# Kernel tuning notes

Hardware: AMD Instinct MI355X
Metric: run time of the kernel (lower is better)

Reference implementation:

```python
import jax, jax.numpy as jnp
import numpy as np

EPS = 1e-12  # F.normalize eps

def _l2norm(v, axis):
    n = jnp.sqrt(jnp.sum(v * v, axis=axis, keepdims=True))
    return v / jnp.maximum(n, EPS)

def setup_inputs() -> dict:
    key = jax.random.key(0)
    k1, k2, k3 = jax.random.split(key, 3)
    B, C, H, W, K = 64, 128, 64, 64, 64
    x = jax.random.normal(k1, (B, C, H, W), dtype=jnp.float32)
    conv_w = jax.random.normal(k2, (K, C), dtype=jnp.float32) * 0.1  # 1x1 conv, no bias
    centroids = jax.random.uniform(k3, (K, C), dtype=jnp.float32)
    return {"x": x, "conv_w": conv_w, "centroids": centroids}

def reference(x, conv_w, centroids):
    B, C, H, W = x.shape
    K = conv_w.shape[0]
    x_flat = x.reshape(B, C, H * W)                     # [B,C,N]
    logits = jnp.einsum('kc,bcn->bkn', conv_w, x_flat)  # 1x1 conv
    a = jax.nn.softmax(logits, axis=1)                  # softmax over clusters
    # vlad[b,k,c] = sum_n a[b,k,n] * (x[b,c,n] - centroids[k,c])
    vlad = jnp.einsum('bkn,bcn->bkc', a, x_flat) - a.sum(axis=2)[:, :, None] * centroids[None]
    vlad = _l2norm(vlad, axis=2)          # intra-normalize per cluster
    vlad = vlad.reshape(B, K * C)
    vlad = _l2norm(vlad, axis=1)          # global L2 normalize
    return vlad
```

## Files before the change

### kernel.cpp

```cpp
#include <hip/hip_runtime.h>
#include <math.h>

#define BB 64
#define CC 128
#define KK 64
#define NN 4096
#define PCH 128
#define NCH 8
#define SLAB (PCH*NCH)
#define VSTRIDE ((size_t)BB*KK*CC)

typedef __attribute__((ext_vector_type(8))) short short8;
typedef __attribute__((ext_vector_type(16))) float f32x16;

__device__ __forceinline__ unsigned f2bf(float f) {
    unsigned u = __float_as_uint(f);
    return (u + 0x7fffu + ((u >> 16) & 1u)) >> 16;
}

__device__ __forceinline__ short8 pack8(float4 a, float4 b) {
    short8 r;
    r[0]=(short)f2bf(a.x); r[1]=(short)f2bf(a.y); r[2]=(short)f2bf(a.z); r[3]=(short)f2bf(a.w);
    r[4]=(short)f2bf(b.x); r[5]=(short)f2bf(b.y); r[6]=(short)f2bf(b.z); r[7]=(short)f2bf(b.w);
    return r;
}

#define LDS_FENCE_BARRIER() do {                                  \
    asm volatile("s_waitcnt lgkmcnt(0)" ::: "memory");            \
    __builtin_amdgcn_s_barrier();                                 \
} while (0)

__global__ __launch_bounds__(512, 2) void nv_phase1(
    const float* __restrict__ x,
    const float* __restrict__ convw,
    float* __restrict__ vlad,
    float* __restrict__ wsf)
{
    __shared__ alignas(16) unsigned short xs[PCH*CC];
    __shared__ alignas(16) unsigned short xc[CC*PCH];
    __shared__ float redsm[2][PCH];
    __shared__ float asred[2][2][16][4];

    unsigned short* al = xs;

    const int t  = threadIdx.x;
    const int b  = blockIdx.y;
    const int slab = blockIdx.x;
    const int n_slab = slab * SLAB;
    const int l   = t & 63;
    const int wid = t >> 6;
    const int ln  = l & 31;
    const int q   = l >> 5;
    const int kt  = wid & 1;
    const int nt  = wid >> 1;
    const int ct  = wid & 3;
    const int kt2 = wid >> 2;
    const int r4  = t & 3;

    const float* xb = x + (size_t)b * CC * NN;
    const int n_ = ln + 32*nt;
    const int c2 = ln + 32*ct;
    const int k2 = ln + 32*kt2;

    float4 pf[8];
#pragma unroll
    for (int i = 0; i < 8; ++i) {
        int u = (t >> 2) + 128 * i, cQ = u >> 5, nQ = u & 31;
        pf[i] = *(const float4*)(xb + (size_t)(4*cQ + r4) * NN + n_slab + 4*nQ);
    }

    short8 wfrag[8];
    {
        const float* wr = convw + (size_t)(ln + 32*kt) * CC + 8*q;
#pragma unroll
        for (int cs = 0; cs < 8; ++cs) {
            float4 a  = *(const float4*)(wr + 16*cs);
            float4 bb = *(const float4*)(wr + 16*cs + 4);
            wfrag[cs] = pack8(a, bb);
        }
    }

    f32x16 vacc;
#pragma unroll
    for (int i = 0; i < 16; ++i) vacc[i] = 0.f;
    float asum_l[16];
#pragma unroll
    for (int i = 0; i < 16; ++i) asum_l[i] = 0.f;

#pragma unroll 1
    for (int chk = 0; chk < NCH; ++chk) {
#pragma unroll
        for (int i = 0; i < 8; ++i) {
            int u = (t >> 2) + 128 * i, cQ = u >> 5, nQ = u & 31;
            unsigned d0 = f2bf(pf[i].x) | (f2bf(pf[i].y) << 16);
            unsigned d1 = f2bf(pf[i].z) | (f2bf(pf[i].w) << 16);
            int c = 4*cQ + r4;
            *(uint2*)((char*)xc + c*256 + ((((nQ >> 1) ^ (c & 7)) << 4) | ((nQ & 1) * 8)))
                = make_uint2(d0, d1);
            unsigned q0 = (unsigned)__shfl_xor((int)d0, 1);
            unsigned q1 = (unsigned)__shfl_xor((int)d1, 1);
            unsigned e, f;
            if (r4 & 1) { e = (q0 >> 16) | (d0 & 0xffff0000u);
                          f = (q1 >> 16) | (d1 & 0xffff0000u); }
            else        { e = (d0 & 0xffffu) | (q0 << 16);
                          f = (d1 & 0xffffu) | (q1 << 16); }
            unsigned s2 = (unsigned)__shfl_xor((int)((r4 & 2) ? e : f), 2);
            unsigned w0 = (r4 & 2) ? s2 : e;
            unsigned w1 = (r4 & 2) ? f : s2;
            int nn  = 4*nQ + r4;
            int chp = (cQ >> 1) ^ (nn & 7);
            *(uint2*)((char*)xs + nn*256 + (chp << 4) + (cQ & 1)*8) = make_uint2(w0, w1);
        }
        if (chk + 1 < NCH) {
            const int gn1 = n_slab + (chk + 1) * PCH;
#pragma unroll
            for (int i = 0; i < 8; ++i) {
                int u = (t >> 2) + 128 * i, cQ = u >> 5, nQ = u & 31;
                pf[i] = *(const float4*)(xb + (size_t)(4*cQ + r4) * NN + gn1 + 4*nQ);
            }
        }
        LDS_FENCE_BARRIER();

        f32x16 lacc;
#pragma unroll
        for (int i = 0; i < 16; ++i) lacc[i] = 0.f;
#pragma unroll
        for (int cs = 0; cs < 8; ++cs) {
            int chp = (2*cs + q) ^ (n_ & 7);
            short8 bf = *(const short8*)((const char*)xs + n_*256 + (chp << 4));
            lacc = __builtin_amdgcn_mfma_f32_32x32x16_bf16(wfrag[cs], bf, lacc, 0, 0, 0);
        }

        float ssum = 0.f;
#pragma unroll
        for (int i = 0; i < 16; ++i) { float e2 = __expf(lacc[i]); lacc[i] = e2; ssum += e2; }
        ssum += __shfl_xor(ssum, 32);
        if (q == 0) redsm[kt][n_] = ssum;
        LDS_FENCE_BARRIER();

        float inv = 1.0f / (redsm[0][n_] + redsm[1][n_]);
#pragma unroll
        for (int i = 0; i < 16; ++i) {
            float a = lacc[i] * inv;
            asum_l[i] += a;
            int k_ = 32*kt + 4*q + (i & 3) + 8*(i >> 2);
            al[k_*128 + ((((n_ >> 3) ^ (k_ & 7)) << 3) | (n_ & 7))] = (unsigned short)f2bf(a);
        }
        LDS_FENCE_BARRIER();

#pragma unroll
        for (int ns = 0; ns < 8; ++ns) {
            int ca = (2*ns + q) ^ (c2 & 7);
            short8 af = *(const short8*)((const char*)xc + c2*256 + (ca << 4));
            int cb = (2*ns + q) ^ (k2 & 7);
            short8 bf = *(const short8*)((const char*)al + k2*256 + (cb << 4));
            vacc = __builtin_amdgcn_mfma_f32_32x32x16_bf16(af, bf, vacc, 0, 0, 0);
        }
        LDS_FENCE_BARRIER();
    }

    {
        float* base = (slab == 0)
            ? vlad + (size_t)b * KK * CC
            : wsf + (size_t)(slab - 1) * VSTRIDE + (size_t)b * KK * CC;
        float* vb = base + (size_t)k2 * CC + 32*ct + 4*q;
#pragma unroll
        for (int g = 0; g < 4; ++g) {
            float4 o;
            o.x = vacc[4*g+0]; o.y = vacc[4*g+1]; o.z = vacc[4*g+2]; o.w = vacc[4*g+3];
            *(float4*)(vb + 8*g) = o;
        }
    }

#pragma unroll
    for (int i = 0; i < 16; ++i) {
        float v = asum_l[i];
        v += __shfl_xor(v, 1);  v += __shfl_xor(v, 2);  v += __shfl_xor(v, 4);
        v += __shfl_xor(v, 8);  v += __shfl_xor(v, 16);
        asum_l[i] = v;
    }
    if (ln == 0) {
#pragma unroll
        for (int i = 0; i < 16; ++i) asred[kt][q][i][nt] = asum_l[i];
    }
    __syncthreads();
    if (t < 64) {
        int kt_ = t >> 5, q_ = (t >> 4) & 1, r_ = t & 15;
        int k_ = 32*kt_ + 4*q_ + (r_ & 3) + 8*(r_ >> 2);
        float s = asred[kt_][q_][r_][0] + asred[kt_][q_][r_][1]
                + asred[kt_][q_][r_][2] + asred[kt_][q_][r_][3];
        wsf[3 * VSTRIDE + (size_t)slab * BB * KK + b * KK + k_] = s;
    }
}

__global__ __launch_bounds__(256) void nv_phase2(
    float* __restrict__ vlad,
    const float* __restrict__ wsf,
    const float* __restrict__ cent)
{
    __shared__ float gred[4];
    const int b    = blockIdx.x;
    const int w    = threadIdx.x >> 6;
    const int lane = threadIdx.x & 63;
    const float* ap = wsf + 3 * VSTRIDE;

    float v[32];
    float gsum = 0.f;
#pragma unroll
    for (int r = 0; r < 16; r++) {
        int k = w * 16 + r;
        float a = ap[0*BB*KK + b*KK + k] + ap[1*BB*KK + b*KK + k]
                + ap[2*BB*KK + b*KK + k] + ap[3*BB*KK + b*KK + k];
        size_t o = ((size_t)b * KK + k) * CC + lane;
        float x0 = vlad[o]      + wsf[o]      + wsf[VSTRIDE + o]      + wsf[2*VSTRIDE + o];
        float x1 = vlad[o + 64] + wsf[o + 64] + wsf[VSTRIDE + o + 64] + wsf[2*VSTRIDE + o + 64];
        x0 -= a * cent[k * CC + lane];
        x1 -= a * cent[k * CC + lane + 64];
        float ss = x0 * x0 + x1 * x1;
#pragma unroll
        for (int m = 1; m < 64; m <<= 1) ss += __shfl_xor(ss, m, 64);
        float rn = 1.0f / fmaxf(sqrtf(ss), 1e-12f);
        v[2 * r]     = x0 * rn;
        v[2 * r + 1] = x1 * rn;
        gsum += ss * rn * rn;
    }
    if (lane == 0) gred[w] = gsum;
    __syncthreads();
    float g  = gred[0] + gred[1] + gred[2] + gred[3];
    float gs = 1.0f / fmaxf(sqrtf(g), 1e-12f);
#pragma unroll
    for (int r = 0; r < 16; r++) {
        int k = w * 16 + r;
        vlad[((size_t)b * KK + k) * CC + lane]      = v[2 * r]     * gs;
        vlad[((size_t)b * KK + k) * CC + lane + 64] = v[2 * r + 1] * gs;
    }
}

extern "C" void kernel_launch(void* const* d_in, const int* in_sizes, int n_in,
                              void* d_out, int out_size, void* d_ws, size_t ws_size,
                              hipStream_t stream) {
    const float* x     = (const float*)d_in[0];
    const float* convw = (const float*)d_in[1];
    const float* cent  = (const float*)d_in[2];
    float* out = (float*)d_out;
    float* wsf = (float*)d_ws;

    nv_phase1<<<dim3(NN / SLAB, BB), 512, 0, stream>>>(x, convw, out, wsf);
    nv_phase2<<<BB, 256, 0, stream>>>(out, wsf, cent);
}
```

Measured before the change: 48.88 us.

## Halve slab length to double phase-1 blocks and fold assignment sums into MFMA loop

Each phase-1 block now covers half as many spatial chunks, so the grid has twice as many blocks (8 slabs per batch) and the occupancy hint is raised to 4 blocks per CU. The per-cluster assignment sums are no longer accumulated in registers and reduced through shared memory at the end; they are summed from the bf16 assignment fragments already loaded for the second MFMA. This removes the tail reduction and its barrier. In exchange there are more partial VLAD slabs written to and read back from the workspace in phase 2, and the assignment sums now come from bf16-rounded values.

```diff
diff --git a/kernel.cpp b/kernel.cpp
--- a/kernel.cpp
+++ b/kernel.cpp
@@ -6,8 +6,9 @@
 #define KK 64
 #define NN 4096
 #define PCH 128
-#define NCH 8
+#define NCH 4
 #define SLAB (PCH*NCH)
+#define NSLAB (NN/SLAB)
 #define VSTRIDE ((size_t)BB*KK*CC)
 
 typedef __attribute__((ext_vector_type(8))) short short8;
@@ -30,7 +31,7 @@
     __builtin_amdgcn_s_barrier();                                 \
 } while (0)
 
-__global__ __launch_bounds__(512, 2) void nv_phase1(
+__global__ __launch_bounds__(512, 4) void nv_phase1(
     const float* __restrict__ x,
     const float* __restrict__ convw,
     float* __restrict__ vlad,
@@ -39,7 +40,6 @@
     __shared__ alignas(16) unsigned short xs[PCH*CC];
     __shared__ alignas(16) unsigned short xc[CC*PCH];
     __shared__ float redsm[2][PCH];
-    __shared__ float asred[2][2][16][4];
 
     unsigned short* al = xs;
 
@@ -83,9 +83,7 @@
     f32x16 vacc;
 #pragma unroll
     for (int i = 0; i < 16; ++i) vacc[i] = 0.f;
-    float asum_l[16];
-#pragma unroll
-    for (int i = 0; i < 16; ++i) asum_l[i] = 0.f;
+    float asacc = 0.f;
 
 #pragma unroll 1
     for (int chk = 0; chk < NCH; ++chk) {
@@ -142,7 +140,6 @@
 #pragma unroll
         for (int i = 0; i < 16; ++i) {
             float a = lacc[i] * inv;
-            asum_l[i] += a;
             int k_ = 32*kt + 4*q + (i & 3) + 8*(i >> 2);
             al[k_*128 + ((((n_ >> 3) ^ (k_ & 7)) << 3) | (n_ & 7))] = (unsigned short)f2bf(a);
         }
@@ -155,6 +152,9 @@
             int cb = (2*ns + q) ^ (k2 & 7);
             short8 bf = *(const short8*)((const char*)al + k2*256 + (cb << 4));
             vacc = __builtin_amdgcn_mfma_f32_32x32x16_bf16(af, bf, vacc, 0, 0, 0);
+#pragma unroll
+            for (int e = 0; e < 8; ++e)
+                asacc += __uint_as_float(((unsigned)(unsigned short)bf[e]) << 16);
         }
         LDS_FENCE_BARRIER();
     }
@@ -172,25 +172,9 @@
         }
     }
 
-#pragma unroll
-    for (int i = 0; i < 16; ++i) {
-        float v = asum_l[i];
-        v += __shfl_xor(v, 1);  v += __shfl_xor(v, 2);  v += __shfl_xor(v, 4);
-        v += __shfl_xor(v, 8);  v += __shfl_xor(v, 16);
-        asum_l[i] = v;
-    }
-    if (ln == 0) {
-#pragma unroll
-        for (int i = 0; i < 16; ++i) asred[kt][q][i][nt] = asum_l[i];
-    }
-    __syncthreads();
-    if (t < 64) {
-        int kt_ = t >> 5, q_ = (t >> 4) & 1, r_ = t & 15;
-        int k_ = 32*kt_ + 4*q_ + (r_ & 3) + 8*(r_ >> 2);
-        float s = asred[kt_][q_][r_][0] + asred[kt_][q_][r_][1]
-                + asred[kt_][q_][r_][2] + asred[kt_][q_][r_][3];
-        wsf[3 * VSTRIDE + (size_t)slab * BB * KK + b * KK + k_] = s;
-    }
+    asacc += __shfl_xor(asacc, 32);
+    if ((wid & 3) == 0 && q == 0)
+        wsf[7 * VSTRIDE + (size_t)slab * BB * KK + b * KK + k2] = asacc;
 }
 
 __global__ __launch_bounds__(256) void nv_phase2(
@@ -202,18 +186,23 @@
     const int b    = blockIdx.x;
     const int w    = threadIdx.x >> 6;
     const int lane = threadIdx.x & 63;
-    const float* ap = wsf + 3 * VSTRIDE;
+    const float* ap = wsf + 7 * VSTRIDE;
 
     float v[32];
     float gsum = 0.f;
 #pragma unroll
     for (int r = 0; r < 16; r++) {
         int k = w * 16 + r;
-        float a = ap[0*BB*KK + b*KK + k] + ap[1*BB*KK + b*KK + k]
-                + ap[2*BB*KK + b*KK + k] + ap[3*BB*KK + b*KK + k];
+        float a = 0.f;
+#pragma unroll
+        for (int s = 0; s < NSLAB; ++s) a += ap[(size_t)s * BB * KK + b * KK + k];
         size_t o = ((size_t)b * KK + k) * CC + lane;
-        float x0 = vlad[o]      + wsf[o]      + wsf[VSTRIDE + o]      + wsf[2*VSTRIDE + o];
-        float x1 = vlad[o + 64] + wsf[o + 64] + wsf[VSTRIDE + o + 64] + wsf[2*VSTRIDE + o + 64];
+        float x0 = vlad[o], x1 = vlad[o + 64];
+#pragma unroll
+        for (int s = 0; s < NSLAB - 1; ++s) {
+            x0 += wsf[(size_t)s * VSTRIDE + o];
+            x1 += wsf[(size_t)s * VSTRIDE + o + 64];
+        }
         x0 -= a * cent[k * CC + lane];
         x1 -= a * cent[k * CC + lane + 64];
         float ss = x0 * x0 + x1 * x1;
@@ -245,6 +234,6 @@
     float* out = (float*)d_out;
     float* wsf = (float*)d_ws;
 
-    nv_phase1<<<dim3(NN / SLAB, BB), 512, 0, stream>>>(x, convw, out, wsf);
+    nv_phase1<<<dim3(NSLAB, BB), 512, 0, stream>>>(x, convw, out, wsf);
     nv_phase2<<<BB, 256, 0, stream>>>(out, wsf, cent);
 }
```

After: 77.97 us. +59.5%, slower.
